# Optimization experiments

Measured on AMD Instinct MI355X. Metric: run time of the kernel, lower is better.

## Reference

```python
import jax, jax.numpy as jnp
import numpy as np

NHEAD = 16
EPS = 1e-5

def layer_norm(x, g, b):
    mu = jnp.mean(x, axis=-1, keepdims=True)
    var = jnp.mean(jnp.square(x - mu), axis=-1, keepdims=True)
    return (x - mu) * jax.lax.rsqrt(var + EPS) * g + b

def setup_inputs() -> dict:
    key = jax.random.key(0)
    ks = jax.random.split(key, 12)
    d_model, d_hid = 1024, 4096  # MHA num_hiddens == dim_feedforward (source quirk)
    B, S = 2, 2048
    s_in = 1.0 / np.sqrt(d_model)
    s_hid = 1.0 / np.sqrt(d_hid)
    return {
        "x": jax.random.normal(ks[0], (B, S, d_model), jnp.float32),
        "Wq": jax.random.normal(ks[1], (d_model, d_hid), jnp.float32) * s_in,
        "Wk": jax.random.normal(ks[2], (d_model, d_hid), jnp.float32) * s_in,
        "Wv": jax.random.normal(ks[3], (d_model, d_hid), jnp.float32) * s_in,
        "Wo": jax.random.normal(ks[4], (d_hid, d_model), jnp.float32) * s_hid,
        "W1": jax.random.normal(ks[5], (d_model, d_hid), jnp.float32) * s_in,
        "b1": jnp.zeros((d_hid,), jnp.float32),
        "W2": jax.random.normal(ks[6], (d_hid, d_model), jnp.float32) * s_hid,
        "b2": jnp.zeros((d_model,), jnp.float32),
        "g1": jnp.ones((d_model,), jnp.float32),
        "be1": jnp.zeros((d_model,), jnp.float32),
        "g2": jnp.ones((d_model,), jnp.float32),
        "be2": jnp.zeros((d_model,), jnp.float32),
    }

def reference(x, Wq, Wk, Wv, Wo, W1, b1, W2, b2, g1, be1, g2, be2):
    B, S, D = x.shape
    H = NHEAD
    # pre-norm attention branch (dropout = identity at eval)
    x1 = layer_norm(x, g1, be1)
    q = (x1 @ Wq).reshape(B, S, H, -1)  # [B,S,H,dh], dh = num_hiddens/H
    k = (x1 @ Wk).reshape(B, S, H, -1)
    v = (x1 @ Wv).reshape(B, S, H, -1)
    dh = q.shape[-1]
    scores = jnp.einsum('bqhd,bkhd->bhqk', q, k) / jnp.sqrt(jnp.float32(dh))
    attn = jax.nn.softmax(scores, axis=-1)
    ctx = jnp.einsum('bhqk,bkhd->bqhd', attn, v).reshape(B, S, -1)
    x = x + ctx @ Wo
    # pre-norm FFN branch
    x2 = layer_norm(x, g2, be2)
    h = jax.nn.relu(x2 @ W1 + b1)
    out = x + (h @ W2 + b2)
    return out
```

## Files before the change

### kernel.cpp

```cpp
#include <hip/hip_runtime.h>
#include <hip/hip_bf16.h>
#include <stdint.h>

using bf16x8 = __attribute__((ext_vector_type(8))) __bf16;
using f32x4  = __attribute__((ext_vector_type(4))) float;

__device__ __forceinline__ uint16_t f2bf(float f) {
    uint32_t u = __builtin_bit_cast(uint32_t, f);
    u += 0x7FFFu + ((u >> 16) & 1u);
    return (uint16_t)(u >> 16);
}
__device__ __forceinline__ uint32_t pack2bf(float lo, float hi) {
    return (uint32_t)f2bf(lo) | ((uint32_t)f2bf(hi) << 16);
}

__device__ __forceinline__ void gld_lds16(const void* g, void* l) {
    __builtin_amdgcn_global_load_lds(
        (const __attribute__((address_space(1))) void*)g,
        (__attribute__((address_space(3))) void*)l,
        16, 0, 0);
}

__global__ __launch_bounds__(256)
void wconv(const float* __restrict__ in, uint16_t* __restrict__ out, int R, int C) {
    __shared__ float t[32][33];
    int c0 = blockIdx.x * 32, r0 = blockIdx.y * 32;
    int tx = threadIdx.x & 31, ty = threadIdx.x >> 5;
    #pragma unroll
    for (int i = 0; i < 32; i += 8)
        t[ty + i][tx] = in[(size_t)(r0 + ty + i) * C + c0 + tx];
    __syncthreads();
    #pragma unroll
    for (int i = 0; i < 32; i += 8)
        out[(size_t)(c0 + ty + i) * R + r0 + tx] = f2bf(t[tx][ty + i]);
}

__global__ __launch_bounds__(256)
void ln_bf16(const float* __restrict__ x, const float* __restrict__ gw,
             const float* __restrict__ bw, uint16_t* __restrict__ out) {
    const int D = 1024;
    int row = blockIdx.x;
    float4 v = ((const float4*)(x + (size_t)row * D))[threadIdx.x];
    float s  = v.x + v.y + v.z + v.w;
    float ss = v.x * v.x + v.y * v.y + v.z * v.z + v.w * v.w;
    #pragma unroll
    for (int m = 1; m < 64; m <<= 1) {
        s  += __shfl_xor(s, m);
        ss += __shfl_xor(ss, m);
    }
    __shared__ float red[8];
    int wid = threadIdx.x >> 6, lane = threadIdx.x & 63;
    if (lane == 0) { red[wid] = s; red[4 + wid] = ss; }
    __syncthreads();
    s  = red[0] + red[1] + red[2] + red[3];
    ss = red[4] + red[5] + red[6] + red[7];
    float mu  = s * (1.f / 1024.f);
    float var = ss * (1.f / 1024.f) - mu * mu;
    float rstd = rsqrtf(var + 1e-5f);
    float4 gv = ((const float4*)gw)[threadIdx.x];
    float4 bv = ((const float4*)bw)[threadIdx.x];
    ushort4 o;
    o.x = f2bf((v.x - mu) * rstd * gv.x + bv.x);
    o.y = f2bf((v.y - mu) * rstd * gv.y + bv.y);
    o.z = f2bf((v.z - mu) * rstd * gv.z + bv.z);
    o.w = f2bf((v.w - mu) * rstd * gv.w + bv.w);
    ((ushort4*)(out + (size_t)row * D))[threadIdx.x] = o;
}

template <int EPI>
__global__ __launch_bounds__(256, 2)
void gemm_bt(const uint16_t* __restrict__ A, const uint16_t* __restrict__ B,
             void* __restrict__ Cp, const float* __restrict__ bias,
             const float* __restrict__ resid, int M, int N, int K) {
    __shared__ uint16_t sA[128 * 32];
    __shared__ uint16_t sB[128 * 32];
    int bid = blockIdx.x;
    int cpx = gridDim.x >> 3;
    bid = (bid & 7) * cpx + (bid >> 3);
    int nbn  = N >> 7;
    int brow = (bid / nbn) << 7;
    int bcol = (bid % nbn) << 7;
    int t = threadIdx.x;
    int wid = t >> 6, lane = t & 63;
    int wr = (wid >> 1) << 6, wc = (wid & 1) << 6;
    int q = lane & 15, g = lane >> 4;

    f32x4 acc[4][4] = {};

    const uint16_t* Abase = A + (size_t)brow * K + ((lane & 3) << 3);
    const uint16_t* Bbase = B + (size_t)bcol * K + ((lane & 3) << 3);
    int rsub = lane >> 2;

    for (int kt = 0; kt < K; kt += 32) {
        __syncthreads();
        #pragma unroll
        for (int i = 0; i < 2; ++i) {
            int chunk = i * 4 + wid;
            int row = chunk * 16 + rsub;
            gld_lds16(Abase + (size_t)row * K + kt, &sA[chunk * 512]);
            gld_lds16(Bbase + (size_t)row * K + kt, &sB[chunk * 512]);
        }
        __syncthreads();
        bf16x8 af[4], bfr[4];
        #pragma unroll
        for (int i = 0; i < 4; ++i)
            af[i] = *(const bf16x8*)&sA[(wr + i * 16 + q) * 32 + g * 8];
        #pragma unroll
        for (int j = 0; j < 4; ++j)
            bfr[j] = *(const bf16x8*)&sB[(wc + j * 16 + q) * 32 + g * 8];
        #pragma unroll
        for (int i = 0; i < 4; ++i)
            #pragma unroll
            for (int j = 0; j < 4; ++j)
                acc[i][j] = __builtin_amdgcn_mfma_f32_16x16x32_bf16(
                    af[i], bfr[j], acc[i][j], 0, 0, 0);
    }

    uint16_t* Cb = (uint16_t*)Cp;
    float*    Cf = (float*)Cp;
    #pragma unroll
    for (int i = 0; i < 4; ++i) {
        #pragma unroll
        for (int j = 0; j < 4; ++j) {
            #pragma unroll
            for (int r = 0; r < 4; ++r) {
                int gr = brow + wr + i * 16 + g * 4 + r;
                int gc = bcol + wc + j * 16 + q;
                float v = acc[i][j][r];
                size_t idx = (size_t)gr * N + gc;
                if constexpr (EPI == 0) {
                    Cb[idx] = f2bf(v);
                } else if constexpr (EPI == 1) {
                    v += bias[gc];
                    Cb[idx] = f2bf(v > 0.f ? v : 0.f);
                } else if constexpr (EPI == 2) {
                    Cf[idx] = v + bias[gc] + resid[idx];
                } else {
                    Cf[idx] = v + resid[idx];
                }
            }
        }
    }
}

__device__ __forceinline__ void attn_stage(uint8_t* smem, int bufsel,
        const uint16_t* Kb0, const uint16_t* Vb0, int ktok, int wid, int lane) {
    #pragma unroll
    for (int i = 0; i < 4; ++i) {
        int chunk = wid * 4 + i;
        int r = 2 * chunk + (lane >> 5);
        int s = lane & 31;
        int cg = (s & ~7) | ((s ^ r) & 7);
        gld_lds16(Kb0 + (size_t)(ktok + r) * 4096 + cg * 8,
                  smem + bufsel * 16384 + chunk * 1024);
    }
    #pragma unroll
    for (int i = 0; i < 4; ++i) {
        int chunk = wid * 4 + i;
        int r = 16 * chunk + (lane >> 2);
        int s = lane & 3;
        int cg = s ^ (r & 3);
        gld_lds16(Vb0 + (size_t)r * 4096 + ktok + cg * 8,
                  smem + 32768 + bufsel * 16384 + chunk * 1024);
    }
}

__device__ __forceinline__ bf16x8 sm_pack(const f32x4* sacc, f32x4* acc,
                                          float& m_run, float& l_run,
                                          int q, int g) {
    float mx = fmaxf(fmaxf(fmaxf(sacc[0][0], sacc[0][1]), fmaxf(sacc[0][2], sacc[0][3])),
                     fmaxf(fmaxf(sacc[1][0], sacc[1][1]), fmaxf(sacc[1][2], sacc[1][3])));
    mx = fmaxf(mx, __shfl_xor(mx, 16));
    mx = fmaxf(mx, __shfl_xor(mx, 32));
    if (!__all(mx - m_run <= 8.f)) {
        float m_new = fmaxf(m_run, mx);
        float alpha = __expf(m_run - m_new);
        l_run *= alpha;
        #pragma unroll
        for (int td = 0; td < 16; ++td) {
            acc[td][0] *= alpha; acc[td][1] *= alpha;
            acc[td][2] *= alpha; acc[td][3] *= alpha;
        }
        m_run = m_new;
    }
    float p[8]; float rs = 0.f;
    #pragma unroll
    for (int tm = 0; tm < 2; ++tm)
        #pragma unroll
        for (int r = 0; r < 4; ++r) {
            float e = __expf(sacc[tm][r] - m_run);
            p[tm * 4 + r] = e; rs += e;
        }
    rs += __shfl_xor(rs, 16);
    rs += __shfl_xor(rs, 32);
    l_run += rs;

    uint32_t pk0 = pack2bf(p[0], p[1]);
    uint32_t pk1 = pack2bf(p[2], p[3]);
    uint32_t pk2 = pack2bf(p[4], p[5]);
    uint32_t pk3 = pack2bf(p[6], p[7]);
    int srcA = ((g & 1) << 5) + q;
    int srcB = srcA + 16;
    uint32_t a0 = __shfl(pk0, srcA), a1 = __shfl(pk2, srcA);
    uint32_t b0 = __shfl(pk1, srcA), b1 = __shfl(pk3, srcA);
    uint32_t c0 = __shfl(pk0, srcB), c1 = __shfl(pk2, srcB);
    uint32_t d0 = __shfl(pk1, srcB), d1 = __shfl(pk3, srcB);
    bool hi = g >= 2;
    uint4 pb;
    pb.x = hi ? a1 : a0;
    pb.y = hi ? b1 : b0;
    pb.z = hi ? c1 : c0;
    pb.w = hi ? d1 : d0;
    return __builtin_bit_cast(bf16x8, pb);
}

__global__ __launch_bounds__(256, 2)
void attn(const uint16_t* __restrict__ Qg, const uint16_t* __restrict__ Kg,
          const uint16_t* __restrict__ Vtg, uint16_t* __restrict__ Og) {
    const int S = 2048, NC = 4096, NT = 64;
    __shared__ uint8_t smem[65536];

    int id = blockIdx.x;
    id = (id & 7) * 64 + (id >> 3);
    int qb = id & 15, h = (id >> 4) & 15, b = id >> 8;

    int t = threadIdx.x;
    int wid = t >> 6, lane = t & 63;
    int q = lane & 15, g = lane >> 4;
    int tok0 = b * S + qb * 128 + wid * 32;

    bf16x8 qf0[8], qf1[8];
    {
        const uint16_t* qrow0 = Qg + (size_t)(tok0 + q) * NC + h * 256 + g * 8;
        const uint16_t* qrow1 = Qg + (size_t)(tok0 + 16 + q) * NC + h * 256 + g * 8;
        #pragma unroll
        for (int c = 0; c < 8; ++c) {
            bf16x8 r0 = *(const bf16x8*)(qrow0 + c * 32);
            bf16x8 r1 = *(const bf16x8*)(qrow1 + c * 32);
            #pragma unroll
            for (int i = 0; i < 8; ++i) {
                r0[i] = (__bf16)((float)r0[i] * 0.0625f);
                r1[i] = (__bf16)((float)r1[i] * 0.0625f);
            }
            qf0[c] = r0; qf1[c] = r1;
        }
    }

    f32x4 acc0[16] = {}, acc1[16] = {};
    float m0 = -1e30f, l0 = 0.f;
    float m1 = -1e30f, l1 = 0.f;

    const uint16_t* Kb0 = Kg + (size_t)(b * S) * NC + h * 256;
    const uint16_t* Vb0 = Vtg + (size_t)(h * 256) * NC + b * S;

    attn_stage(smem, 0, Kb0, Vb0, 0, wid, lane);

    for (int kt = 0; kt < NT; ++kt) {
        int cb = (kt & 1) * 16384;
        if (kt + 1 < NT) {
            attn_stage(smem, (kt + 1) & 1, Kb0, Vb0, (kt + 1) * 32, wid, lane);
            asm volatile("s_waitcnt vmcnt(8)" ::: "memory");
        } else {
            asm volatile("s_waitcnt vmcnt(0)" ::: "memory");
        }
        __builtin_amdgcn_sched_barrier(0);
        __builtin_amdgcn_s_barrier();

        const uint16_t* sk = (const uint16_t*)(smem + cb);
        const uint16_t* sv = (const uint16_t*)(smem + 32768 + cb);

        f32x4 sA0[2] = {}, sA1[2] = {};
        __builtin_amdgcn_s_setprio(1);
        #pragma unroll
        for (int c = 0; c < 8; ++c) {
            #pragma unroll
            for (int tm = 0; tm < 2; ++tm) {
                int G = c * 4 + g;
                int slot = (G & ~7) | ((G ^ q) & 7);
                bf16x8 kf = *(const bf16x8*)(sk + (tm * 16 + q) * 256 + slot * 8);
                sA0[tm] = __builtin_amdgcn_mfma_f32_16x16x32_bf16(kf, qf0[c], sA0[tm], 0, 0, 0);
                sA1[tm] = __builtin_amdgcn_mfma_f32_16x16x32_bf16(kf, qf1[c], sA1[tm], 0, 0, 0);
            }
        }
        __builtin_amdgcn_s_setprio(0);

        bf16x8 pfrag0 = sm_pack(sA0, acc0, m0, l0, q, g);
        bf16x8 pfrag1 = sm_pack(sA1, acc1, m1, l1, q, g);

        int sl = g ^ (q & 3);
        __builtin_amdgcn_s_setprio(1);
        #pragma unroll
        for (int td = 0; td < 16; ++td) {
            bf16x8 vf = *(const bf16x8*)(sv + (td * 16 + q) * 32 + sl * 8);
            acc0[td] = __builtin_amdgcn_mfma_f32_16x16x32_bf16(vf, pfrag0, acc0[td], 0, 0, 0);
            acc1[td] = __builtin_amdgcn_mfma_f32_16x16x32_bf16(vf, pfrag1, acc1[td], 0, 0, 0);
        }
        __builtin_amdgcn_s_setprio(0);
        __builtin_amdgcn_s_barrier();
    }

    __syncthreads();
    {
        float inv0 = 1.f / l0, inv1 = 1.f / l1;
        uint32_t* w0 = (uint32_t*)(smem + wid * 16384);
        uint32_t* w1 = (uint32_t*)(smem + wid * 16384 + 8192);
        #pragma unroll
        for (int td = 0; td < 16; ++td) {
            int base = (q * 256 + td * 16 + g * 4) >> 1;
            w0[base]     = pack2bf(acc0[td][0] * inv0, acc0[td][1] * inv0);
            w0[base + 1] = pack2bf(acc0[td][2] * inv0, acc0[td][3] * inv0);
            w1[base]     = pack2bf(acc1[td][0] * inv1, acc1[td][1] * inv1);
            w1[base + 1] = pack2bf(acc1[td][2] * inv1, acc1[td][3] * inv1);
        }
    }
    __syncthreads();
    #pragma unroll
    for (int s2 = 0; s2 < 2; ++s2) {
        const uint16_t* tb = (const uint16_t*)(smem + wid * 16384 + s2 * 8192);
        #pragma unroll
        for (int r2 = 0; r2 < 8; ++r2) {
            int c = r2 * 64 + lane;
            int qq = c >> 5, dc = c & 31;
            uint4 v = *(const uint4*)&tb[qq * 256 + dc * 8];
            *(uint4*)(Og + (size_t)(tok0 + s2 * 16 + qq) * NC + h * 256 + dc * 8) = v;
        }
    }
}

extern "C" void kernel_launch(void* const* d_in, const int* in_sizes, int n_in,
                              void* d_out, int out_size, void* d_ws, size_t ws_size,
                              hipStream_t stream) {
    const float* x   = (const float*)d_in[0];
    const float* Wq  = (const float*)d_in[1];
    const float* Wk  = (const float*)d_in[2];
    const float* Wv  = (const float*)d_in[3];
    const float* Wo  = (const float*)d_in[4];
    const float* W1  = (const float*)d_in[5];
    const float* b1  = (const float*)d_in[6];
    const float* W2  = (const float*)d_in[7];
    const float* b2  = (const float*)d_in[8];
    const float* g1  = (const float*)d_in[9];
    const float* be1 = (const float*)d_in[10];
    const float* g2  = (const float*)d_in[11];
    const float* be2 = (const float*)d_in[12];

    char* ws = (char*)d_ws;
    const size_t M8 = 8388608;
    uint16_t* WqT  = (uint16_t*)(ws + 0 * M8);
    uint16_t* WkT  = (uint16_t*)(ws + 1 * M8);
    uint16_t* WvT  = (uint16_t*)(ws + 2 * M8);
    uint16_t* WoT  = (uint16_t*)(ws + 3 * M8);
    uint16_t* W1T  = (uint16_t*)(ws + 4 * M8);
    uint16_t* W2T  = (uint16_t*)(ws + 5 * M8);
    uint16_t* x1   = (uint16_t*)(ws + 6 * M8);
    uint16_t* x2   = (uint16_t*)(ws + 7 * M8);
    uint16_t* Q    = (uint16_t*)(ws + 8 * M8);
    uint16_t* Kq   = (uint16_t*)(ws + 12 * M8);
    uint16_t* Vt   = (uint16_t*)(ws + 16 * M8);
    uint16_t* ctx  = (uint16_t*)(ws + 20 * M8);
    float*    xmid = (float*)(ws + 12 * M8);
    uint16_t* Hn   = (uint16_t*)(ws + 8 * M8);

    wconv<<<dim3(128, 32), 256, 0, stream>>>(Wq, WqT, 1024, 4096);
    wconv<<<dim3(128, 32), 256, 0, stream>>>(Wk, WkT, 1024, 4096);
    wconv<<<dim3(128, 32), 256, 0, stream>>>(Wv, WvT, 1024, 4096);
    wconv<<<dim3(32, 128), 256, 0, stream>>>(Wo, WoT, 4096, 1024);
    wconv<<<dim3(128, 32), 256, 0, stream>>>(W1, W1T, 1024, 4096);
    wconv<<<dim3(32, 128), 256, 0, stream>>>(W2, W2T, 4096, 1024);

    ln_bf16<<<4096, 256, 0, stream>>>(x, g1, be1, x1);

    gemm_bt<0><<<1024, 256, 0, stream>>>(x1, WqT, Q,  nullptr, nullptr, 4096, 4096, 1024);
    gemm_bt<0><<<1024, 256, 0, stream>>>(x1, WkT, Kq, nullptr, nullptr, 4096, 4096, 1024);
    gemm_bt<0><<<1024, 256, 0, stream>>>(WvT, x1, Vt, nullptr, nullptr, 4096, 4096, 1024);

    attn<<<512, 256, 0, stream>>>(Q, Kq, Vt, ctx);

    gemm_bt<3><<<256, 256, 0, stream>>>(ctx, WoT, xmid, nullptr, x, 4096, 1024, 4096);

    ln_bf16<<<4096, 256, 0, stream>>>(xmid, g2, be2, x2);

    gemm_bt<1><<<1024, 256, 0, stream>>>(x2, W1T, Hn, b1, nullptr, 4096, 4096, 1024);
    gemm_bt<2><<<256, 256, 0, stream>>>(Hn, W2T, d_out, b2, xmid, 4096, 1024, 4096);
}
```

Before: 539.6 us.

## Add 256x256-tile double-buffered GEMM kernel for the bf16-output projections

Adds a new GEMM kernel with 256x256 output tiles, 512 threads, and a BK=64 double-buffered LDS pipeline that overlaps global-to-LDS loads with MFMA. It uses XOR-swizzled LDS layouts, an XCD-aware block remap, and raised wave priority during MFMA. The QKV and FFN1 GEMMs switch to this kernel, while the old kernel keeps only the fp32 residual epilogues. The goal is more data reuse per tile and hidden load latency. The cost is fewer blocks (256), 128KB of LDS per block, and higher register pressure.

```diff
diff --git a/kernel.cpp b/kernel.cpp
--- a/kernel.cpp
+++ b/kernel.cpp
@@ -116,8 +116,7 @@
                     af[i], bfr[j], acc[i][j], 0, 0, 0);
     }
 
-    uint16_t* Cb = (uint16_t*)Cp;
-    float*    Cf = (float*)Cp;
+    float* Cf = (float*)Cp;
     #pragma unroll
     for (int i = 0; i < 4; ++i) {
         #pragma unroll
@@ -128,12 +127,7 @@
                 int gc = bcol + wc + j * 16 + q;
                 float v = acc[i][j][r];
                 size_t idx = (size_t)gr * N + gc;
-                if constexpr (EPI == 0) {
-                    Cb[idx] = f2bf(v);
-                } else if constexpr (EPI == 1) {
-                    v += bias[gc];
-                    Cb[idx] = f2bf(v > 0.f ? v : 0.f);
-                } else if constexpr (EPI == 2) {
+                if constexpr (EPI == 2) {
                     Cf[idx] = v + bias[gc] + resid[idx];
                 } else {
                     Cf[idx] = v + resid[idx];
@@ -141,6 +135,120 @@
             }
         }
     }
+}
+
+template <int EPI>
+__global__ __launch_bounds__(512, 2)
+void gemm256(const uint16_t* __restrict__ A, const uint16_t* __restrict__ B,
+             void* __restrict__ Cp, const float* __restrict__ bias,
+             int M, int N, int K) {
+    __shared__ uint8_t smem[131072];
+    int bid = blockIdx.x;
+    int cpx = gridDim.x >> 3;
+    bid = (bid & 7) * cpx + (bid >> 3);
+    int nbn  = N >> 8;
+    int brow = (bid / nbn) << 8;
+    int bcol = (bid % nbn) << 8;
+    int t0 = threadIdx.x;
+    int wid = t0 >> 6, lane = t0 & 63;
+    int wr = wid >> 2, wc = wid & 3;
+    int q = lane & 15, g = lane >> 4;
+
+    const uint16_t* Asw = A + (size_t)(brow + (lane >> 3)) * K + (((lane & 7) ^ (lane >> 3)) << 3);
+    const uint16_t* Bsw = B + (size_t)(bcol + (lane >> 3)) * K + (((lane & 7) ^ (lane >> 3)) << 3);
+
+    f32x4 acc[2][2][4][2] = {};
+    int NKT = K >> 6;
+
+#define STAGE256(BSEL, KK)                                                     \
+    {                                                                          \
+        uint8_t* dA = smem + (BSEL) * 32768;                                   \
+        uint8_t* dB = smem + 65536 + (BSEL) * 32768;                           \
+        _Pragma("unroll")                                                      \
+        for (int i = 0; i < 4; ++i) {                                          \
+            int c = wid * 4 + i;                                               \
+            gld_lds16(Asw + (size_t)(c * 8) * K + (KK), dA + c * 1024);        \
+            gld_lds16(Bsw + (size_t)(c * 8) * K + (KK), dB + c * 1024);        \
+        }                                                                      \
+    }
+
+    STAGE256(0, 0)
+
+    for (int t = 0; t < NKT; ++t) {
+        int cur = t & 1;
+        if (t + 1 < NKT) {
+            STAGE256(cur ^ 1, (t + 1) << 6)
+            asm volatile("s_waitcnt vmcnt(8)" ::: "memory");
+        } else {
+            asm volatile("s_waitcnt vmcnt(0)" ::: "memory");
+        }
+        __builtin_amdgcn_sched_barrier(0);
+        __builtin_amdgcn_s_barrier();
+        __builtin_amdgcn_sched_barrier(0);
+
+        const uint8_t* bA = smem + cur * 32768;
+        const uint8_t* bB = smem + 65536 + cur * 32768;
+
+        bf16x8 af[4][2], bfr[2][2];
+
+#define LOADA256(MH)                                                           \
+        _Pragma("unroll")                                                      \
+        for (int m2 = 0; m2 < 4; ++m2)                                         \
+            _Pragma("unroll")                                                  \
+            for (int ks = 0; ks < 2; ++ks) {                                   \
+                int rr = wr * 128 + (MH) * 64 + m2 * 16 + q;                   \
+                int sl = (ks * 4 + g) ^ (q & 7);                               \
+                af[m2][ks] = *(const bf16x8*)(bA + rr * 128 + sl * 16);        \
+            }
+#define LOADB256(NH)                                                           \
+        _Pragma("unroll")                                                      \
+        for (int n2 = 0; n2 < 2; ++n2)                                         \
+            _Pragma("unroll")                                                  \
+            for (int ks = 0; ks < 2; ++ks) {                                   \
+                int cc = wc * 64 + (NH) * 32 + n2 * 16 + q;                    \
+                int sl = (ks * 4 + g) ^ (q & 7);                               \
+                bfr[n2][ks] = *(const bf16x8*)(bB + cc * 128 + sl * 16);       \
+            }
+#define MMQ256(MH, NH)                                                         \
+        __builtin_amdgcn_s_setprio(1);                                         \
+        _Pragma("unroll")                                                      \
+        for (int m2 = 0; m2 < 4; ++m2)                                         \
+            _Pragma("unroll")                                                  \
+            for (int n2 = 0; n2 < 2; ++n2)                                     \
+                _Pragma("unroll")                                              \
+                for (int ks = 0; ks < 2; ++ks)                                 \
+                    acc[MH][NH][m2][n2] = __builtin_amdgcn_mfma_f32_16x16x32_bf16( \
+                        af[m2][ks], bfr[n2][ks], acc[MH][NH][m2][n2], 0, 0, 0);\
+        __builtin_amdgcn_s_setprio(0);
+
+        LOADA256(0) LOADB256(0) MMQ256(0, 0)
+        LOADB256(1) MMQ256(0, 1)
+        LOADA256(1) MMQ256(1, 1)
+        LOADB256(0) MMQ256(1, 0)
+
+        __builtin_amdgcn_s_barrier();
+    }
+
+    uint16_t* Cb = (uint16_t*)Cp;
+    #pragma unroll
+    for (int mh = 0; mh < 2; ++mh)
+        #pragma unroll
+        for (int nh = 0; nh < 2; ++nh)
+            #pragma unroll
+            for (int m2 = 0; m2 < 4; ++m2)
+                #pragma unroll
+                for (int n2 = 0; n2 < 2; ++n2)
+                    #pragma unroll
+                    for (int r = 0; r < 4; ++r) {
+                        int gr = brow + wr * 128 + mh * 64 + m2 * 16 + g * 4 + r;
+                        int gc = bcol + wc * 64 + nh * 32 + n2 * 16 + q;
+                        float v = acc[mh][nh][m2][n2][r];
+                        if constexpr (EPI == 1) {
+                            v += bias[gc];
+                            v = v > 0.f ? v : 0.f;
+                        }
+                        Cb[(size_t)gr * N + gc] = f2bf(v);
+                    }
 }
 
 __device__ __forceinline__ void attn_stage(uint8_t* smem, int bufsel,
@@ -370,9 +478,9 @@
 
     ln_bf16<<<4096, 256, 0, stream>>>(x, g1, be1, x1);
 
-    gemm_bt<0><<<1024, 256, 0, stream>>>(x1, WqT, Q,  nullptr, nullptr, 4096, 4096, 1024);
-    gemm_bt<0><<<1024, 256, 0, stream>>>(x1, WkT, Kq, nullptr, nullptr, 4096, 4096, 1024);
-    gemm_bt<0><<<1024, 256, 0, stream>>>(WvT, x1, Vt, nullptr, nullptr, 4096, 4096, 1024);
+    gemm256<0><<<256, 512, 0, stream>>>(x1, WqT, Q,  nullptr, 4096, 4096, 1024);
+    gemm256<0><<<256, 512, 0, stream>>>(x1, WkT, Kq, nullptr, 4096, 4096, 1024);
+    gemm256<0><<<256, 512, 0, stream>>>(WvT, x1, Vt, nullptr, 4096, 4096, 1024);
 
     attn<<<512, 256, 0, stream>>>(Q, Kq, Vt, ctx);
 
@@ -380,6 +488,6 @@
 
     ln_bf16<<<4096, 256, 0, stream>>>(xmid, g2, be2, x2);
 
-    gemm_bt<1><<<1024, 256, 0, stream>>>(x2, W1T, Hn, b1, nullptr, 4096, 4096, 1024);
+    gemm256<1><<<256, 512, 0, stream>>>(x2, W1T, Hn, b1, 4096, 4096, 1024);
     gemm_bt<2><<<256, 256, 0, stream>>>(Hn, W2T, d_out, b2, xmid, 4096, 1024, 4096);
 }
```

Result: faster. 520.5 us (-3.5%).
